# Kernel tuning notes

Measured on AMD Instinct MI355X. Metric: run time of the kernel, lower is better.

The kernel has to match this reference:

```python
import jax, jax.numpy as jnp
import numpy as np

V, D, DEPTH, L, H, DH, FF = 32000, 1024, 4, 2048, 16, 64, 4096
INNER = H * DH
EPS = 1e-5


def ln(x, g, b):
    m = jnp.mean(x, axis=-1, keepdims=True)
    v = jnp.mean(jnp.square(x - m), axis=-1, keepdims=True)
    return (x - m) * jax.lax.rsqrt(v + EPS) * g + b


def setup_inputs() -> dict:
    key = jax.random.key(0)
    ks = jax.random.split(key, 16)
    s = 0.02
    inp = {
        'x': jax.random.randint(ks[0], (1, L), 0, V),
        'tok_emb': jax.random.normal(ks[1], (V, D), jnp.float32) * s,
        'pos_emb': jax.random.normal(ks[2], (L, D), jnp.float32) * s,
        'attn_ng': jnp.ones((DEPTH, D), jnp.float32),
        'attn_nb': jnp.zeros((DEPTH, D), jnp.float32),
        'wqkv': jax.random.normal(ks[3], (DEPTH, D, 3 * INNER), jnp.float32) * s,
        'wo': jax.random.normal(ks[4], (DEPTH, INNER, D), jnp.float32) * s,
        'bo': jnp.zeros((DEPTH, D), jnp.float32),
        'out_ng': jnp.ones((DEPTH, D), jnp.float32),
        'out_nb': jnp.zeros((DEPTH, D), jnp.float32),
        'ff_ng': jnp.ones((DEPTH, D), jnp.float32),
        'ff_nb': jnp.zeros((DEPTH, D), jnp.float32),
        'w1': jax.random.normal(ks[5], (DEPTH, D, FF), jnp.float32) * s,
        'b1': jnp.zeros((DEPTH, FF), jnp.float32),
        'w2': jax.random.normal(ks[6], (DEPTH, FF, D), jnp.float32) * s,
        'b2': jnp.zeros((DEPTH, D), jnp.float32),
        'fin_g': jnp.ones((D,), jnp.float32),
        'fin_b': jnp.zeros((D,), jnp.float32),
        'w_logit': jax.random.normal(ks[7], (D, V), jnp.float32) * s,
        'b_logit': jnp.zeros((V,), jnp.float32),
    }
    return inp


def reference(x, tok_emb, pos_emb, attn_ng, attn_nb, wqkv, wo, bo, out_ng, out_nb,
              ff_ng, ff_nb, w1, b1, w2, b2, fin_g, fin_b, w_logit, b_logit):
    n = x.shape[1]
    scale = DH ** -0.5
    # causal keep-mask: j <= i (lower triangular incl diagonal)
    causal = jnp.tril(jnp.ones((n, n), bool))
    h = tok_emb[x] + pos_emb[:n][None]  # [b, n, D]
    for l in range(DEPTH):
        # --- ReLA attention ---
        y = ln(h, attn_ng[l], attn_nb[l])
        qkv = y @ wqkv[l]  # [b, n, 3*INNER]
        q, k, v = jnp.split(qkv, 3, axis=-1)
        q = q.reshape(-1, n, H, DH).transpose(0, 2, 1, 3) * scale  # [b,H,n,d]
        k = k.reshape(-1, n, H, DH).transpose(0, 2, 1, 3)
        v = v.reshape(-1, n, H, DH).transpose(0, 2, 1, 3)
        sim = jnp.einsum('bhid,bhjd->bhij', q, k)
        attn = jnp.where(causal, jax.nn.relu(sim), 0.0)  # mask then ReLU
        o = jnp.einsum('bhij,bhjd->bhid', attn, v)
        o = o.transpose(0, 2, 1, 3).reshape(-1, n, INNER)  # [b,n,INNER]
        o = ln(o @ wo[l] + bo[l], out_ng[l], out_nb[l])
        h = o + h
        # --- FFN ---
        y = ln(h, ff_ng[l], ff_nb[l])
        y = jax.nn.gelu(y @ w1[l] + b1[l], approximate=False) @ w2[l] + b2[l]
        h = y + h
    return ln(h, fin_g, fin_b) @ w_logit + b_logit
```

## Files before the change

### kernel.cpp

```cpp
#include <hip/hip_runtime.h>
#include <hip/hip_bf16.h>
#include <math.h>

#define SEQ   2048
#define DM    1024
#define NH    16
#define DHD   64
#define FFD   4096
#define NV    32000

typedef __bf16 bf16x8 __attribute__((ext_vector_type(8)));
typedef float  f32x4  __attribute__((ext_vector_type(4)));

typedef __attribute__((address_space(1))) void* gas_ptr;
typedef __attribute__((address_space(3))) void* las_ptr;

static __device__ __forceinline__ void gload16(const void* g, void* l) {
  __builtin_amdgcn_global_load_lds((gas_ptr)g, (las_ptr)l, 16, 0, 0);
}

static __device__ __forceinline__ unsigned short f2bf(float f) {
  unsigned int x = __float_as_uint(f);
  return (unsigned short)((x + 0x7fffu + ((x >> 16) & 1u)) >> 16);
}

static __device__ __forceinline__ bf16x8 ld_frag(const unsigned short* p) {
  union { uint4 u; bf16x8 v; } r;
  r.u = *(const uint4*)p;
  return r.v;
}

__global__ __launch_bounds__(256)
void k_transpose_bf16(const float* __restrict__ in, unsigned short* __restrict__ out,
                      int K, int N, size_t lstride) {
  in  += (size_t)blockIdx.z * lstride;
  out += (size_t)blockIdx.z * lstride;
  __shared__ float tl[64 * 65];
  const int bk = blockIdx.x * 64, bn = blockIdx.y * 64;
  const int t = threadIdx.x;
  const int tx = t & 15, ty = t >> 4;
#pragma unroll
  for (int i = 0; i < 4; ++i) {
    const int r = i * 16 + ty;
    float4 v = *(const float4*)&in[(size_t)(bk + r) * N + bn + tx * 4];
    tl[(tx * 4 + 0) * 65 + r] = v.x;
    tl[(tx * 4 + 1) * 65 + r] = v.y;
    tl[(tx * 4 + 2) * 65 + r] = v.z;
    tl[(tx * 4 + 3) * 65 + r] = v.w;
  }
  __syncthreads();
#pragma unroll
  for (int j = 0; j < 2; ++j) {
    const int f = j * 256 + t;
    const int n = f >> 3, kc = (f & 7) * 8;
    union { unsigned short u[8]; uint4 v; } pk;
#pragma unroll
    for (int e = 0; e < 8; ++e) pk.u[e] = f2bf(tl[n * 65 + kc + e]);
    *(uint4*)&out[(size_t)(bn + n) * K + bk + kc] = pk.v;
  }
}

__global__ __launch_bounds__(256)
void k_vT(const unsigned short* __restrict__ qkv, unsigned short* __restrict__ vT) {
  __shared__ unsigned short tile[32][33];
  const int bs = blockIdx.x * 32, bd = blockIdx.y * 32;
  const int tx = threadIdx.x & 31, ty = threadIdx.x >> 5;
#pragma unroll
  for (int r = ty; r < 32; r += 8)
    tile[r][tx] = qkv[(size_t)(bs + r) * (3 * DM) + 2 * DM + bd + tx];
  __syncthreads();
#pragma unroll
  for (int r = ty; r < 32; r += 8)
    vT[(size_t)(bd + r) * SEQ + bs + tx] = tile[tx][r];
}

__global__ __launch_bounds__(256)
void k_embed(const int* __restrict__ x, const float* __restrict__ tok,
             const float* __restrict__ pos, float* __restrict__ h) {
  const int row = blockIdx.x;
  const int d = threadIdx.x * 4;
  const int tk = x[row];
  float4 a = *(const float4*)(tok + (size_t)tk * DM + d);
  float4 p = *(const float4*)(pos + (size_t)row * DM + d);
  float4 o; o.x = a.x + p.x; o.y = a.y + p.y; o.z = a.z + p.z; o.w = a.w + p.w;
  *(float4*)(h + (size_t)row * DM + d) = o;
}

__global__ __launch_bounds__(256)
void k_ln_bf16(const float* __restrict__ in, const float* __restrict__ g,
               const float* __restrict__ b, unsigned short* __restrict__ out) {
  const int row = blockIdx.x, t = threadIdx.x;
  float4 v = *(const float4*)(in + (size_t)row * DM + t * 4);
  float s = v.x + v.y + v.z + v.w;
  float q = v.x * v.x + v.y * v.y + v.z * v.z + v.w * v.w;
#pragma unroll
  for (int o = 32; o; o >>= 1) { s += __shfl_xor(s, o); q += __shfl_xor(q, o); }
  __shared__ float ls[4], lq[4];
  if ((t & 63) == 0) { ls[t >> 6] = s; lq[t >> 6] = q; }
  __syncthreads();
  s = ls[0] + ls[1] + ls[2] + ls[3];
  q = lq[0] + lq[1] + lq[2] + lq[3];
  const float mean = s * (1.f / DM);
  const float rstd = rsqrtf(q * (1.f / DM) - mean * mean + 1e-5f);
  float4 gg = *(const float4*)(g + t * 4);
  float4 bb = *(const float4*)(b + t * 4);
  ushort4 o4;
  o4.x = f2bf((v.x - mean) * rstd * gg.x + bb.x);
  o4.y = f2bf((v.y - mean) * rstd * gg.y + bb.y);
  o4.z = f2bf((v.z - mean) * rstd * gg.z + bb.z);
  o4.w = f2bf((v.w - mean) * rstd * gg.w + bb.w);
  *(ushort4*)(out + (size_t)row * DM + t * 4) = o4;
}

__global__ __launch_bounds__(256)
void k_add_ln_ln(float* __restrict__ h, const float* __restrict__ in,
                 const float* __restrict__ g1, const float* __restrict__ b1,
                 const float* __restrict__ g2, const float* __restrict__ b2,
                 unsigned short* __restrict__ out) {
  const int row = blockIdx.x, t = threadIdx.x;
  __shared__ float ls[4], lq[4], ls2[4], lq2[4];
  float4 v = *(const float4*)(in + (size_t)row * DM + t * 4);
  float s = v.x + v.y + v.z + v.w;
  float q = v.x * v.x + v.y * v.y + v.z * v.z + v.w * v.w;
#pragma unroll
  for (int o = 32; o; o >>= 1) { s += __shfl_xor(s, o); q += __shfl_xor(q, o); }
  if ((t & 63) == 0) { ls[t >> 6] = s; lq[t >> 6] = q; }
  __syncthreads();
  s = ls[0] + ls[1] + ls[2] + ls[3];
  q = lq[0] + lq[1] + lq[2] + lq[3];
  const float mean = s * (1.f / DM);
  const float rstd = rsqrtf(q * (1.f / DM) - mean * mean + 1e-5f);
  float4 gg = *(const float4*)(g1 + t * 4);
  float4 bb = *(const float4*)(b1 + t * 4);
  float4 hv = *(const float4*)(h + (size_t)row * DM + t * 4);
  hv.x += (v.x - mean) * rstd * gg.x + bb.x;
  hv.y += (v.y - mean) * rstd * gg.y + bb.y;
  hv.z += (v.z - mean) * rstd * gg.z + bb.z;
  hv.w += (v.w - mean) * rstd * gg.w + bb.w;
  *(float4*)(h + (size_t)row * DM + t * 4) = hv;
  float s2 = hv.x + hv.y + hv.z + hv.w;
  float q2 = hv.x * hv.x + hv.y * hv.y + hv.z * hv.z + hv.w * hv.w;
#pragma unroll
  for (int o = 32; o; o >>= 1) { s2 += __shfl_xor(s2, o); q2 += __shfl_xor(q2, o); }
  if ((t & 63) == 0) { ls2[t >> 6] = s2; lq2[t >> 6] = q2; }
  __syncthreads();
  s2 = ls2[0] + ls2[1] + ls2[2] + ls2[3];
  q2 = lq2[0] + lq2[1] + lq2[2] + lq2[3];
  const float mean2 = s2 * (1.f / DM);
  const float rstd2 = rsqrtf(q2 * (1.f / DM) - mean2 * mean2 + 1e-5f);
  float4 g2v = *(const float4*)(g2 + t * 4);
  float4 b2v = *(const float4*)(b2 + t * 4);
  ushort4 o4;
  o4.x = f2bf((hv.x - mean2) * rstd2 * g2v.x + b2v.x);
  o4.y = f2bf((hv.y - mean2) * rstd2 * g2v.y + b2v.y);
  o4.z = f2bf((hv.z - mean2) * rstd2 * g2v.z + b2v.z);
  o4.w = f2bf((hv.w - mean2) * rstd2 * g2v.w + b2v.w);
  *(ushort4*)(out + (size_t)row * DM + t * 4) = o4;
}

__global__ __launch_bounds__(256)
void k_red_add(float* __restrict__ h, const float* __restrict__ sl,
               const float* __restrict__ b2) {
  const int row = blockIdx.x, d = threadIdx.x * 4;
  const size_t idx = (size_t)row * DM + d;
  float4 hv = *(const float4*)(h + idx);
  float4 bb = *(const float4*)(b2 + d);
  hv.x += bb.x; hv.y += bb.y; hv.z += bb.z; hv.w += bb.w;
#pragma unroll
  for (int c = 0; c < 4; ++c) {
    float4 p = *(const float4*)(sl + (size_t)c * SEQ * DM + idx);
    hv.x += p.x; hv.y += p.y; hv.z += p.z; hv.w += p.w;
  }
  *(float4*)(h + idx) = hv;
}

template<int EPI>
__global__ __launch_bounds__(512, 1)
void k_gemm2(const unsigned short* __restrict__ A, const unsigned short* __restrict__ Bt,
             float* __restrict__ outF, unsigned short* __restrict__ outB,
             const float* __restrict__ bias, int N, int K, int kLen, int gm) {
  __shared__ __align__(16) unsigned short L[49152];
  const int nwg = gridDim.x, pid = blockIdx.x;
  const int qq = nwg >> 3, rr = nwg & 7;
  const int xcd = pid & 7, lo = pid >> 3;
  const int wg = ((xcd < rr) ? xcd * (qq + 1) : rr * (qq + 1) + (xcd - rr) * qq) + lo;
  const int bm = wg % gm, bn = wg / gm;
  const int kOff = blockIdx.y * kLen;
  const int t = threadIdx.x, lane = t & 63, w = t >> 6;
  const int wm = w >> 2, wn = w & 3, lr = lane & 15, lg = lane >> 4;

  const unsigned short* gA[2]; unsigned short* lA[2];
  const unsigned short* gB[4]; unsigned short* lB[4];
#pragma unroll
  for (int j = 0; j < 2; ++j) {
    const int f = j * 512 + t, row = f >> 3, c = f & 7;
    gA[j] = A + (size_t)(bm * 128 + row) * K + kOff + ((c ^ (row & 7)) << 3);
    lA[j] = L + f * 8;
  }
#pragma unroll
  for (int j = 0; j < 4; ++j) {
    const int f = j * 512 + t, row = f >> 3, c = f & 7;
    gB[j] = Bt + (size_t)(bn * 256 + row) * K + kOff + ((c ^ (row & 7)) << 3);
    lB[j] = L + 16384 + f * 8;
  }
  auto stage = [&](int k0, int c) {
#pragma unroll
    for (int j = 0; j < 2; ++j) gload16(gA[j] + k0, lA[j] + c * 8192);
#pragma unroll
    for (int j = 0; j < 4; ++j) gload16(gB[j] + k0, lB[j] + c * 16384);
  };

  int offA[4][2], offB[4][2];
#pragma unroll
  for (int mt = 0; mt < 4; ++mt)
#pragma unroll
    for (int ks = 0; ks < 2; ++ks) {
      const int rowA = wm * 64 + mt * 16 + lr;
      offA[mt][ks] = rowA * 64 + (((ks * 4 + lg) ^ (rowA & 7)) << 3);
      const int rowB = wn * 64 + mt * 16 + lr;
      offB[mt][ks] = rowB * 64 + (((ks * 4 + lg) ^ (rowB & 7)) << 3);
    }

  const f32x4 zero = {0.f, 0.f, 0.f, 0.f};
  f32x4 acc[4][4];
#pragma unroll
  for (int i = 0; i < 4; ++i)
#pragma unroll
    for (int j = 0; j < 4; ++j) acc[i][j] = zero;

  const int NT = kLen >> 6;
  stage(0, 0);
  if (NT > 1) stage(64, 1);

  for (int tt = 0; tt < NT; ++tt) {
    const int c = tt & 1;
    if (tt + 1 < NT) asm volatile("s_waitcnt vmcnt(6)" ::: "memory");
    else             asm volatile("s_waitcnt vmcnt(0)" ::: "memory");
    __builtin_amdgcn_s_barrier();
    const unsigned short* Ab = L + c * 8192;
    const unsigned short* Bb = L + 16384 + c * 16384;
    bf16x8 af[4][2], bfr[4][2];
#pragma unroll
    for (int mt = 0; mt < 4; ++mt)
#pragma unroll
      for (int ks = 0; ks < 2; ++ks) {
        af[mt][ks]  = ld_frag(Ab + offA[mt][ks]);
        bfr[mt][ks] = ld_frag(Bb + offB[mt][ks]);
      }
    __builtin_amdgcn_s_setprio(1);
#pragma unroll
    for (int mt = 0; mt < 4; ++mt)
#pragma unroll
      for (int nt = 0; nt < 4; ++nt)
#pragma unroll
        for (int ks = 0; ks < 2; ++ks)
          acc[mt][nt] = __builtin_amdgcn_mfma_f32_16x16x32_bf16(af[mt][ks], bfr[nt][ks], acc[mt][nt], 0, 0, 0);
    __builtin_amdgcn_s_setprio(0);
    asm volatile("s_waitcnt lgkmcnt(0)" ::: "memory");
    __builtin_amdgcn_s_barrier();
    if (tt + 2 < NT) stage((tt + 2) << 6, c);
  }

  const int rbase = bm * 128 + wm * 64;
  const int cbase = bn * 256 + wn * 64;
  float* outP = outF;
  if constexpr (EPI == 4) outP = outF + (size_t)blockIdx.y * SEQ * N;
#pragma unroll
  for (int mt = 0; mt < 4; ++mt) {
#pragma unroll
    for (int nt = 0; nt < 4; ++nt) {
      const int col = cbase + nt * 16 + lr;
      float bv = 0.f;
      if constexpr (EPI == 1 || EPI == 2) bv = bias[col];
#pragma unroll
      for (int r = 0; r < 4; ++r) {
        const int row = rbase + mt * 16 + lg * 4 + r;
        float v = acc[mt][nt][r] + bv;
        if constexpr (EPI == 2) v = 0.5f * v * (1.f + erff(v * 0.70710678118f));
        if constexpr (EPI == 0 || EPI == 2) outB[(size_t)row * N + col] = f2bf(v);
        else                                outP[(size_t)row * N + col] = v;
      }
    }
  }
}

__global__ __launch_bounds__(512, 1)
void k_gemm3(const unsigned short* __restrict__ A, const unsigned short* __restrict__ Bt,
             float* __restrict__ outF, const float* __restrict__ bias,
             int N, int K, int gm) {
  __shared__ __align__(16) unsigned short L[65536];
  const int nwg = gridDim.x, pid = blockIdx.x;
  const int qq = nwg >> 3, rr = nwg & 7;
  const int xcd = pid & 7, lo = pid >> 3;
  const int wg = ((xcd < rr) ? xcd * (qq + 1) : rr * (qq + 1) + (xcd - rr) * qq) + lo;
  const int bm = wg % gm, bn = wg / gm;
  const int t = threadIdx.x, lane = t & 63, w = t >> 6;
  const int wm = w >> 2, wn = w & 3, lr = lane & 15, lg = lane >> 4;
  const int NT = K >> 6;

  int offA[8][2], offB[4][2];
#pragma unroll
  for (int mt = 0; mt < 8; ++mt) {
    const int row = mt * 32 + wm * 16 + lr;
#pragma unroll
    for (int ks = 0; ks < 2; ++ks)
      offA[mt][ks] = row * 64 + (((ks * 4 + lg) ^ (row & 7)) << 3);
  }
#pragma unroll
  for (int nt = 0; nt < 4; ++nt) {
    const int row = ((nt & 1) << 6) + ((nt >> 1) << 7) + wn * 16 + lr;
#pragma unroll
    for (int ks = 0; ks < 2; ++ks)
      offB[nt][ks] = 16384 + row * 64 + (((ks * 4 + lg) ^ (row & 7)) << 3);
  }

  const unsigned short* gA = A  + (size_t)(bm * 256) * K;
  const unsigned short* gB = Bt + (size_t)(bn * 256) * K;

  auto stage_half = [&](int which, int tile, int half) {
    const int tt = (tile < NT) ? tile : (NT - 1);
    const unsigned short* g = which ? gB : gA;
    const int bufo = (tile & 1) << 15;
#pragma unroll
    for (int j = 0; j < 2; ++j) {
      const int f = (j << 9) + t;
      const int r = (half << 7) + (f >> 3);
      const int c = (f & 7) ^ (r & 7);
      gload16(g + (size_t)r * K + (tt << 6) + (c << 3),
              L + bufo + (which << 14) + (half << 13) + f * 8);
    }
  };

  f32x4 acc[8][4];
#pragma unroll
  for (int i = 0; i < 8; ++i)
#pragma unroll
    for (int j = 0; j < 4; ++j) acc[i][j] = (f32x4){0.f, 0.f, 0.f, 0.f};
  bf16x8 af[4][2], bfr[2][2];

  stage_half(1, 0, 0); stage_half(0, 0, 1); stage_half(0, 0, 0);
  stage_half(1, 0, 1); stage_half(1, 1, 0); stage_half(0, 1, 1);

#define PHASE(VMS, LDA, LDB, MH, NH, BUFO, SW, ST, SH) do {                    \
  asm volatile("s_waitcnt vmcnt(" VMS ")" ::: "memory");                       \
  __builtin_amdgcn_s_barrier();                                                \
  if (LDA) {                                                                   \
    _Pragma("unroll") for (int mt = 0; mt < 4; ++mt)                           \
    _Pragma("unroll") for (int ks = 0; ks < 2; ++ks)                           \
      af[mt][ks] = ld_frag(L + (BUFO) + offA[(MH) * 4 + mt][ks]);              \
  }                                                                            \
  if (LDB) {                                                                   \
    _Pragma("unroll") for (int n = 0; n < 2; ++n)                              \
    _Pragma("unroll") for (int ks = 0; ks < 2; ++ks)                           \
      bfr[n][ks] = ld_frag(L + (BUFO) + offB[(NH) * 2 + n][ks]);               \
  }                                                                            \
  stage_half((SW), (ST), (SH));                                                \
  asm volatile("s_waitcnt lgkmcnt(0)" ::: "memory");                           \
  __builtin_amdgcn_sched_barrier(0);                                           \
  __builtin_amdgcn_s_setprio(1);                                               \
  _Pragma("unroll") for (int mt = 0; mt < 4; ++mt)                             \
  _Pragma("unroll") for (int n = 0; n < 2; ++n)                                \
  _Pragma("unroll") for (int ks = 0; ks < 2; ++ks)                             \
    acc[(MH) * 4 + mt][(NH) * 2 + n] = __builtin_amdgcn_mfma_f32_16x16x32_bf16(\
        af[mt][ks], bfr[n][ks], acc[(MH) * 4 + mt][(NH) * 2 + n], 0, 0, 0);    \
  __builtin_amdgcn_s_setprio(0);                                               \
} while (0)

  for (int I = 0; I < (NT >> 1); ++I) {
    const int T = I << 1;
    PHASE("4", 1, 1, 0, 0, 0,     0, T + 1, 0);
    PHASE("8", 1, 0, 1, 0, 0,     1, T + 1, 1);
    PHASE("6", 0, 1, 1, 1, 0,     1, T + 2, 0);
    PHASE("8", 1, 0, 0, 1, 0,     0, T + 2, 1);
    PHASE("4", 1, 1, 0, 0, 32768, 0, T + 2, 0);
    PHASE("8", 1, 0, 1, 0, 32768, 1, T + 2, 1);
    PHASE("6", 0, 1, 1, 1, 32768, 1, T + 3, 0);
    PHASE("8", 1, 0, 0, 1, 32768, 0, T + 3, 1);
  }
#undef PHASE

#pragma unroll
  for (int mt = 0; mt < 8; ++mt) {
    const int row0 = bm * 256 + mt * 32 + wm * 16 + lg * 4;
#pragma unroll
    for (int nt = 0; nt < 4; ++nt) {
      const int col = bn * 256 + ((nt & 1) << 6) + ((nt >> 1) << 7) + wn * 16 + lr;
      const float bv = bias[col];
#pragma unroll
      for (int r = 0; r < 4; ++r)
        outF[(size_t)(row0 + r) * N + col] = acc[mt][nt][r] + bv;
    }
  }
}

__global__ __launch_bounds__(256)
void k_rela_attn(const unsigned short* __restrict__ qkv,
                 const unsigned short* __restrict__ vT,
                 unsigned short* __restrict__ obf) {
  const int jb = blockIdx.x;
  const int hd = blockIdx.y;
  const int qbA = jb, qbB = 31 - jb;
  const int t = threadIdx.x, lane = t & 63, w = t >> 6;
  const int lr = lane & 15, lg = lane >> 4;

  __shared__ __align__(16) unsigned short Qs[128 * 64];
  __shared__ __align__(16) unsigned short Ks[64 * 64];
  __shared__ __align__(16) unsigned short Vs[64 * 64];
  __shared__ __align__(16) unsigned short Ps[4][16 * 72];

  const int sr8 = lane >> 3;
  const int sch = ((lane & 7) ^ sr8) << 3;

#pragma unroll
  for (int qi = 0; qi < 4; ++qi) {
    const int i = w * 4 + qi;
    const int rl = i * 8 + sr8;
    const int grow = (rl < 64) ? (qbA * 64 + rl) : (qbB * 64 + rl - 64);
    gload16(qkv + (size_t)grow * (3 * DM) + hd * DHD + sch, Qs + i * 512);
  }
  __syncthreads();

  bf16x8 qfA[2], qfB[2];
#pragma unroll
  for (int ks = 0; ks < 2; ++ks) {
    const int rowA = w * 16 + lr;
    qfA[ks] = ld_frag(&Qs[rowA * 64 + (((ks * 4 + lg) ^ (lr & 7)) << 3)]);
    const int rowB = 64 + w * 16 + lr;
    qfB[ks] = ld_frag(&Qs[rowB * 64 + (((ks * 4 + lg) ^ (lr & 7)) << 3)]);
  }

  const f32x4 zero = {0.f, 0.f, 0.f, 0.f};
  f32x4 accA[4], accB[4];
#pragma unroll
  for (int nt = 0; nt < 4; ++nt) { accA[nt] = zero; accB[nt] = zero; }

  auto tile_step = [&](const bf16x8* qf, f32x4* acc, int qb, int kt) {
    f32x4 sv[4];
#pragma unroll
    for (int nt = 0; nt < 4; ++nt) sv[nt] = zero;
#pragma unroll
    for (int ks = 0; ks < 2; ++ks)
#pragma unroll
      for (int nt = 0; nt < 4; ++nt) {
        bf16x8 kf = ld_frag(&Ks[(nt * 16 + lr) * 64 + (((ks * 4 + lg) ^ (lr & 7)) << 3)]);
        sv[nt] = __builtin_amdgcn_mfma_f32_16x16x32_bf16(qf[ks], kf, sv[nt], 0, 0, 0);
      }
    const bool diag = (kt == qb);
#pragma unroll
    for (int nt = 0; nt < 4; ++nt)
#pragma unroll
      for (int r = 0; r < 4; ++r) {
        float v = fmaxf(sv[nt][r], 0.f) * 0.125f;
        if (diag) {
          const int ii = w * 16 + lg * 4 + r;
          const int jj = nt * 16 + lr;
          if (jj > ii) v = 0.f;
        }
        Ps[w][(lg * 4 + r) * 72 + nt * 16 + lr] = f2bf(v);
      }
#pragma unroll
    for (int ks = 0; ks < 2; ++ks) {
      bf16x8 pf = ld_frag(&Ps[w][lr * 72 + ks * 32 + lg * 8]);
#pragma unroll
      for (int nt = 0; nt < 4; ++nt) {
        bf16x8 vf = ld_frag(&Vs[(nt * 16 + lr) * 64 + (((ks * 4 + lg) ^ (lr & 7)) << 3)]);
        acc[nt] = __builtin_amdgcn_mfma_f32_16x16x32_bf16(pf, vf, acc[nt], 0, 0, 0);
      }
    }
  };

  for (int kt = 0; kt <= qbB; ++kt) {
    __syncthreads();
#pragma unroll
    for (int qi = 0; qi < 2; ++qi) {
      const int i = w * 2 + qi;
      const int rl = i * 8 + sr8;
      gload16(qkv + (size_t)(kt * 64 + rl) * (3 * DM) + DM + hd * DHD + sch, Ks + i * 512);
      gload16(vT + (size_t)(hd * DHD + rl) * SEQ + kt * 64 + sch, Vs + i * 512);
    }
    __syncthreads();
    tile_step(qfB, accB, qbB, kt);
    if (kt <= qbA) tile_step(qfA, accA, qbA, kt);
  }

#pragma unroll
  for (int nt = 0; nt < 4; ++nt)
#pragma unroll
    for (int r = 0; r < 4; ++r) {
      const int col = hd * DHD + nt * 16 + lr;
      const int rowA = qbA * 64 + w * 16 + lg * 4 + r;
      obf[(size_t)rowA * DM + col] = f2bf(accA[nt][r]);
      const int rowB = qbB * 64 + w * 16 + lg * 4 + r;
      obf[(size_t)rowB * DM + col] = f2bf(accB[nt][r]);
    }
}

extern "C" void kernel_launch(void* const* d_in, const int* in_sizes, int n_in,
                              void* d_out, int out_size, void* d_ws, size_t ws_size,
                              hipStream_t stream) {
  const int*   x       = (const int*)d_in[0];
  const float* tok_emb = (const float*)d_in[1];
  const float* pos_emb = (const float*)d_in[2];
  const float* attn_ng = (const float*)d_in[3];
  const float* attn_nb = (const float*)d_in[4];
  const float* wqkv    = (const float*)d_in[5];
  const float* wo      = (const float*)d_in[6];
  const float* bo      = (const float*)d_in[7];
  const float* out_ng  = (const float*)d_in[8];
  const float* out_nb  = (const float*)d_in[9];
  const float* ff_ng   = (const float*)d_in[10];
  const float* ff_nb   = (const float*)d_in[11];
  const float* w1      = (const float*)d_in[12];
  const float* b1      = (const float*)d_in[13];
  const float* w2      = (const float*)d_in[14];
  const float* b2      = (const float*)d_in[15];
  const float* fin_g   = (const float*)d_in[16];
  const float* fin_b   = (const float*)d_in[17];
  const float* w_logit = (const float*)d_in[18];
  const float* b_logit = (const float*)d_in[19];
  float* out = (float*)d_out;

  char* ws = (char*)d_ws;
  size_t off = 0;
  auto alloc = [&](size_t bytes) -> void* {
    void* p = ws + off;
    off = (off + bytes + 255) & ~(size_t)255;
    return p;
  };
  unsigned short* wqkvT = (unsigned short*)alloc(4ull * 3072 * 1024 * 2);
  unsigned short* woT   = (unsigned short*)alloc(4ull * 1024 * 1024 * 2);
  unsigned short* w1T   = (unsigned short*)alloc(4ull * 4096 * 1024 * 2);
  unsigned short* w2T   = (unsigned short*)alloc(4ull * 1024 * 4096 * 2);
  unsigned short* wlogT = (unsigned short*)alloc((size_t)NV * 1024 * 2);
  float*          h     = (float*)alloc((size_t)SEQ * DM * 4);
  unsigned short* ybf   = (unsigned short*)alloc((size_t)SEQ * DM * 2);
  unsigned short* qkvbf = (unsigned short*)alloc((size_t)SEQ * 3 * DM * 2);
  unsigned short* vTb   = (unsigned short*)alloc((size_t)DM * SEQ * 2);
  unsigned short* obf   = (unsigned short*)alloc((size_t)SEQ * DM * 2);
  float*          tmpf  = (float*)alloc((size_t)SEQ * DM * 4);
  unsigned short* ffbf  = (unsigned short*)alloc((size_t)SEQ * FFD * 2);
  float*          slabs = (float*)alloc(4ull * SEQ * DM * 4);
  (void)ws_size; (void)in_sizes; (void)n_in; (void)out_size;

  const dim3 B(256);
  const dim3 G2(512);

  k_transpose_bf16<<<dim3(16, 48, 4), B, 0, stream>>>(wqkv, wqkvT, 1024, 3072, (size_t)1024 * 3072);
  k_transpose_bf16<<<dim3(16, 16, 4), B, 0, stream>>>(wo, woT, 1024, 1024, (size_t)1024 * 1024);
  k_transpose_bf16<<<dim3(16, 64, 4), B, 0, stream>>>(w1, w1T, 1024, 4096, (size_t)1024 * 4096);
  k_transpose_bf16<<<dim3(64, 16, 4), B, 0, stream>>>(w2, w2T, 4096, 1024, (size_t)4096 * 1024);
  k_transpose_bf16<<<dim3(16, 500, 1), B, 0, stream>>>(w_logit, wlogT, 1024, NV, 0);

  k_embed<<<SEQ, B, 0, stream>>>(x, tok_emb, pos_emb, h);

  for (int l = 0; l < 4; ++l) {
    k_ln_bf16<<<SEQ, B, 0, stream>>>(h, attn_ng + l * DM, attn_nb + l * DM, ybf);
    k_gemm2<0><<<dim3(192), G2, 0, stream>>>(
        ybf, wqkvT + (size_t)l * 3072 * 1024, nullptr, qkvbf, nullptr, 3072, 1024, 1024, 16);
    k_vT<<<dim3(SEQ / 32, DM / 32), B, 0, stream>>>(qkvbf, vTb);
    k_rela_attn<<<dim3(16, NH), B, 0, stream>>>(qkvbf, vTb, obf);
    k_gemm2<1><<<dim3(64), G2, 0, stream>>>(
        obf, woT + (size_t)l * 1024 * 1024, tmpf, nullptr, bo + l * DM, 1024, 1024, 1024, 16);
    k_add_ln_ln<<<SEQ, B, 0, stream>>>(h, tmpf, out_ng + l * DM, out_nb + l * DM,
                                       ff_ng + l * DM, ff_nb + l * DM, ybf);
    k_gemm2<2><<<dim3(256), G2, 0, stream>>>(
        ybf, w1T + (size_t)l * 4096 * 1024, nullptr, ffbf, b1 + l * FFD, 4096, 1024, 1024, 16);
    k_gemm2<4><<<dim3(64, 4), G2, 0, stream>>>(
        ffbf, w2T + (size_t)l * 1024 * 4096, slabs, nullptr, nullptr, 1024, 4096, 1024, 16);
    k_red_add<<<SEQ, B, 0, stream>>>(h, slabs, b2 + l * DM);
  }

  k_ln_bf16<<<SEQ, B, 0, stream>>>(h, fin_g, fin_b, ybf);
  k_gemm3<<<dim3(1000), G2, 0, stream>>>(ybf, wlogT, out, b_logit, NV, 1024, 8);
}
```

Before: 1.140 ms.

## Restructure logit GEMM pipeline with quarter-tile staging and contiguous warp tiles

Rewrites the 256x256 logit GEMM's main loop to stage A/B tiles in 64-row quarters with precomputed per-thread global pointers. It changes each warp's sub-tile to a contiguous 128x64 block and adds a barrier at the end of each phase along with a revised vmcnt wait schedule. The kernel is templated on an epilogue mode so it can later serve the bf16 and GELU outputs, but only the fp32+bias mode is launched. The aim is better overlap of global-to-LDS loads with MFMA work and less address arithmetic, at the cost of extra barriers per phase.

```diff
diff --git a/kernel.cpp b/kernel.cpp
--- a/kernel.cpp
+++ b/kernel.cpp
@@ -284,10 +284,11 @@
   }
 }
 
+template<int EPI>
 __global__ __launch_bounds__(512, 1)
 void k_gemm3(const unsigned short* __restrict__ A, const unsigned short* __restrict__ Bt,
-             float* __restrict__ outF, const float* __restrict__ bias,
-             int N, int K, int gm) {
+             float* __restrict__ outF, unsigned short* __restrict__ outB,
+             const float* __restrict__ bias, int N, int K, int gm) {
   __shared__ __align__(16) unsigned short L[65536];
   const int nwg = gridDim.x, pid = blockIdx.x;
   const int qq = nwg >> 3, rr = nwg & 7;
@@ -298,97 +299,108 @@
   const int wm = w >> 2, wn = w & 3, lr = lane & 15, lg = lane >> 4;
   const int NT = K >> 6;
 
-  int offA[8][2], offB[4][2];
-#pragma unroll
-  for (int mt = 0; mt < 8; ++mt) {
-    const int row = mt * 32 + wm * 16 + lr;
-#pragma unroll
-    for (int ks = 0; ks < 2; ++ks)
-      offA[mt][ks] = row * 64 + (((ks * 4 + lg) ^ (row & 7)) << 3);
-  }
-#pragma unroll
-  for (int nt = 0; nt < 4; ++nt) {
-    const int row = ((nt & 1) << 6) + ((nt >> 1) << 7) + wn * 16 + lr;
-#pragma unroll
-    for (int ks = 0; ks < 2; ++ks)
-      offB[nt][ks] = 16384 + row * 64 + (((ks * 4 + lg) ^ (row & 7)) << 3);
-  }
-
   const unsigned short* gA = A  + (size_t)(bm * 256) * K;
   const unsigned short* gB = Bt + (size_t)(bn * 256) * K;
-
-  auto stage_half = [&](int which, int tile, int half) {
-    const int tt = (tile < NT) ? tile : (NT - 1);
-    const unsigned short* g = which ? gB : gA;
-    const int bufo = (tile & 1) << 15;
-#pragma unroll
-    for (int j = 0; j < 2; ++j) {
-      const int f = (j << 9) + t;
-      const int r = (half << 7) + (f >> 3);
-      const int c = (f & 7) ^ (r & 7);
-      gload16(g + (size_t)r * K + (tt << 6) + (c << 3),
-              L + bufo + (which << 14) + (half << 13) + f * 8);
-    }
+  const int rowLow = t >> 3;
+  const int colOff = ((t & 7) ^ ((t >> 3) & 7)) << 3;
+  const unsigned short* pA = gA + (size_t)rowLow * K + colOff;
+  const unsigned short* pB = gB + (size_t)rowLow * K + colOff;
+  unsigned short* const ldst = L + t * 8;
+
+  auto stageQ = [&](int which, int s, int q) {
+    const int ss = (s < NT) ? s : (NT - 1);
+    const unsigned short* g = (which ? pB : pA) + (size_t)(q * 64) * K + (ss << 6);
+    gload16(g, ldst + ((s & 1) << 15) + (which << 14) + (q << 12));
   };
 
+  int offA[2][4][2], offB[2][2][2];
+#pragma unroll
+  for (int mh = 0; mh < 2; ++mh)
+#pragma unroll
+    for (int mt = 0; mt < 4; ++mt)
+#pragma unroll
+      for (int ks = 0; ks < 2; ++ks) {
+        const int row = wm * 128 + mh * 64 + mt * 16 + lr;
+        offA[mh][mt][ks] = row * 64 + (((ks * 4 + lg) ^ (row & 7)) << 3);
+      }
+#pragma unroll
+  for (int nh = 0; nh < 2; ++nh)
+#pragma unroll
+    for (int n2 = 0; n2 < 2; ++n2)
+#pragma unroll
+      for (int ks = 0; ks < 2; ++ks) {
+        const int row = wn * 64 + nh * 32 + n2 * 16 + lr;
+        offB[nh][n2][ks] = 16384 + row * 64 + (((ks * 4 + lg) ^ (row & 7)) << 3);
+      }
+
   f32x4 acc[8][4];
 #pragma unroll
   for (int i = 0; i < 8; ++i)
 #pragma unroll
     for (int j = 0; j < 4; ++j) acc[i][j] = (f32x4){0.f, 0.f, 0.f, 0.f};
-  bf16x8 af[4][2], bfr[2][2];
-
-  stage_half(1, 0, 0); stage_half(0, 0, 1); stage_half(0, 0, 0);
-  stage_half(1, 0, 1); stage_half(1, 1, 0); stage_half(0, 1, 1);
-
-#define PHASE(VMS, LDA, LDB, MH, NH, BUFO, SW, ST, SH) do {                    \
-  asm volatile("s_waitcnt vmcnt(" VMS ")" ::: "memory");                       \
-  __builtin_amdgcn_s_barrier();                                                \
-  if (LDA) {                                                                   \
-    _Pragma("unroll") for (int mt = 0; mt < 4; ++mt)                           \
-    _Pragma("unroll") for (int ks = 0; ks < 2; ++ks)                           \
-      af[mt][ks] = ld_frag(L + (BUFO) + offA[(MH) * 4 + mt][ks]);              \
-  }                                                                            \
-  if (LDB) {                                                                   \
-    _Pragma("unroll") for (int n = 0; n < 2; ++n)                              \
-    _Pragma("unroll") for (int ks = 0; ks < 2; ++ks)                           \
-      bfr[n][ks] = ld_frag(L + (BUFO) + offB[(NH) * 2 + n][ks]);               \
-  }                                                                            \
-  stage_half((SW), (ST), (SH));                                                \
-  asm volatile("s_waitcnt lgkmcnt(0)" ::: "memory");                           \
-  __builtin_amdgcn_sched_barrier(0);                                           \
-  __builtin_amdgcn_s_setprio(1);                                               \
-  _Pragma("unroll") for (int mt = 0; mt < 4; ++mt)                             \
-  _Pragma("unroll") for (int n = 0; n < 2; ++n)                                \
-  _Pragma("unroll") for (int ks = 0; ks < 2; ++ks)                             \
-    acc[(MH) * 4 + mt][(NH) * 2 + n] = __builtin_amdgcn_mfma_f32_16x16x32_bf16(\
-        af[mt][ks], bfr[n][ks], acc[(MH) * 4 + mt][(NH) * 2 + n], 0, 0, 0);    \
-  __builtin_amdgcn_s_setprio(0);                                               \
+  bf16x8 afA[4][2], bf[2][2][2];
+
+  stageQ(0, 0, 0); stageQ(0, 0, 1); stageQ(0, 0, 2); stageQ(0, 0, 3);
+  stageQ(1, 0, 0); stageQ(1, 0, 1); stageQ(1, 0, 2); stageQ(1, 0, 3);
+  stageQ(0, 1, 0); stageQ(0, 1, 2); stageQ(1, 1, 0); stageQ(1, 1, 1);
+  stageQ(0, 1, 1); stageQ(0, 1, 3);
+  asm volatile("s_waitcnt vmcnt(6)" ::: "memory");
+  __builtin_amdgcn_s_barrier();
+
+#define PH(BUFO, MH, NHq, RDA, RDB, SW, SS, Q1, Q2, VM) do {                    \
+  if (RDA) {                                                                    \
+    _Pragma("unroll") for (int mt = 0; mt < 4; ++mt)                            \
+    _Pragma("unroll") for (int ks = 0; ks < 2; ++ks)                            \
+      afA[mt][ks] = ld_frag(L + (BUFO) + offA[MH][mt][ks]);                     \
+  }                                                                             \
+  if (RDB) {                                                                    \
+    _Pragma("unroll") for (int n2 = 0; n2 < 2; ++n2)                            \
+    _Pragma("unroll") for (int ks = 0; ks < 2; ++ks)                            \
+      bf[NHq][n2][ks] = ld_frag(L + (BUFO) + offB[NHq][n2][ks]);                \
+  }                                                                             \
+  stageQ(SW, SS, Q1); stageQ(SW, SS, Q2);                                       \
+  if (VM) asm volatile("s_waitcnt vmcnt(6)" ::: "memory");                      \
+  __builtin_amdgcn_s_barrier();                                                 \
+  asm volatile("s_waitcnt lgkmcnt(0)" ::: "memory");                            \
+  __builtin_amdgcn_sched_barrier(0);                                            \
+  __builtin_amdgcn_s_setprio(1);                                                \
+  _Pragma("unroll") for (int mt = 0; mt < 4; ++mt)                              \
+  _Pragma("unroll") for (int n2 = 0; n2 < 2; ++n2)                              \
+  _Pragma("unroll") for (int ks = 0; ks < 2; ++ks)                              \
+    acc[(MH) * 4 + mt][(NHq) * 2 + n2] = __builtin_amdgcn_mfma_f32_16x16x32_bf16(\
+        afA[mt][ks], bf[NHq][n2][ks], acc[(MH) * 4 + mt][(NHq) * 2 + n2], 0, 0, 0);\
+  __builtin_amdgcn_s_setprio(0);                                                \
+  __builtin_amdgcn_s_barrier();                                                 \
 } while (0)
 
-  for (int I = 0; I < (NT >> 1); ++I) {
-    const int T = I << 1;
-    PHASE("4", 1, 1, 0, 0, 0,     0, T + 1, 0);
-    PHASE("8", 1, 0, 1, 0, 0,     1, T + 1, 1);
-    PHASE("6", 0, 1, 1, 1, 0,     1, T + 2, 0);
-    PHASE("8", 1, 0, 0, 1, 0,     0, T + 2, 1);
-    PHASE("4", 1, 1, 0, 0, 32768, 0, T + 2, 0);
-    PHASE("8", 1, 0, 1, 0, 32768, 1, T + 2, 1);
-    PHASE("6", 0, 1, 1, 1, 32768, 1, T + 3, 0);
-    PHASE("8", 1, 0, 0, 1, 32768, 0, T + 3, 1);
-  }
-#undef PHASE
-
-#pragma unroll
-  for (int mt = 0; mt < 8; ++mt) {
-    const int row0 = bm * 256 + mt * 32 + wm * 16 + lg * 4;
-#pragma unroll
-    for (int nt = 0; nt < 4; ++nt) {
-      const int col = bn * 256 + ((nt & 1) << 6) + ((nt >> 1) << 7) + wn * 16 + lr;
-      const float bv = bias[col];
-#pragma unroll
-      for (int r = 0; r < 4; ++r)
-        outF[(size_t)(row0 + r) * N + col] = acc[mt][nt][r] + bv;
+  for (int i = 0; i < (NT >> 1); ++i) {
+    const int T0 = 2 * i, T1 = 2 * i + 1;
+    PH(0,     0, 0, 1, 1, 1, T0 + 1, 2, 3, 0);
+    PH(0,     0, 1, 0, 1, 0, T0 + 2, 0, 2, 0);
+    PH(0,     1, 0, 1, 0, 1, T0 + 2, 0, 1, 0);
+    PH(0,     1, 1, 0, 0, 0, T0 + 2, 1, 3, 1);
+    PH(32768, 0, 0, 1, 1, 1, T1 + 1, 2, 3, 0);
+    PH(32768, 0, 1, 0, 1, 0, T1 + 2, 0, 2, 0);
+    PH(32768, 1, 0, 1, 0, 1, T1 + 2, 0, 1, 0);
+    PH(32768, 1, 1, 0, 0, 0, T1 + 2, 1, 3, 1);
+  }
+#undef PH
+
+#pragma unroll
+  for (int ai = 0; ai < 8; ++ai) {
+    const int row0 = bm * 256 + wm * 128 + (ai >> 2) * 64 + (ai & 3) * 16 + lg * 4;
+#pragma unroll
+    for (int bj = 0; bj < 4; ++bj) {
+      const int col = bn * 256 + wn * 64 + (bj >> 1) * 32 + (bj & 1) * 16 + lr;
+      float bv = 0.f;
+      if constexpr (EPI == 1 || EPI == 2) bv = bias[col];
+#pragma unroll
+      for (int r = 0; r < 4; ++r) {
+        float v = acc[ai][bj][r] + bv;
+        if constexpr (EPI == 2) v = 0.5f * v * (1.f + erff(v * 0.70710678118f));
+        if constexpr (EPI == 0 || EPI == 2) outB[(size_t)(row0 + r) * N + col] = f2bf(v);
+        else                                outF[(size_t)(row0 + r) * N + col] = v;
+      }
     }
   }
 }
@@ -571,5 +583,5 @@
   }
 
   k_ln_bf16<<<SEQ, B, 0, stream>>>(h, fin_g, fin_b, ybf);
-  k_gemm3<<<dim3(1000), G2, 0, stream>>>(ybf, wlogT, out, b_logit, NV, 1024, 8);
-}
+  k_gemm3<1><<<dim3(1000), G2, 0, stream>>>(ybf, wlogT, out, nullptr, b_logit, NV, 1024, 8);
+}
```

Result: faster. 1.087 ms (-4.7%).
